# Kernel tuning notes

Hardware: AMD Instinct MI355X
Metric: run time of the kernel (lower is better)

## Reference

```python
import jax, jax.numpy as jnp
import numpy as np

H2 = 1.0  # self.bandwidth = bandwidth**2 with bandwidth=1.0

Q, N, D = 4096, 65536, 32


def setup_inputs() -> dict:
    key = jax.random.key(0)
    k1, k2, k3 = jax.random.split(key, 3)
    X = jax.random.normal(k1, (Q, D), dtype=jnp.float32)
    X_train = jax.random.normal(k2, (N, D), dtype=jnp.float32)
    sample_weight = jax.random.uniform(k3, (N,), dtype=jnp.float32)  # non-negative
    return {"X": X, "X_train": X_train, "sample_weight": sample_weight}


def reference(X, X_train, sample_weight):
    # Brute-force ('standard'/RootTree) KDE: every query sees all train points.
    d = X.shape[-1]
    d2 = (jnp.sum(X * X, axis=-1, keepdims=True)
          + jnp.sum(X_train * X_train, axis=-1)[None, :]
          - 2.0 * (X @ X_train.T))
    # GaussianKernel(diff) = (2*pi)^{-d/2} exp(-||diff||^2 / (2*H2))
    log_k = -0.5 * d2 / H2 - 0.5 * d * jnp.log(jnp.float32(2.0 * np.pi))
    # log( sum_j w_j K_ij / (bw_norm * sum_j w_j) ), bw_norm = H2**(d/2)
    log_num = jax.scipy.special.logsumexp(log_k + jnp.log(sample_weight)[None, :], axis=-1)
    log_norm = 0.5 * d * jnp.log(jnp.float32(H2)) + jnp.log(jnp.sum(sample_weight))
    return log_num - log_norm
```

## Files before the change

kernel.cpp:

```cpp
#include <hip/hip_runtime.h>
#include <math.h>

#define QN 4096
#define NN 65536
#define DD 32

typedef __attribute__((ext_vector_type(8))) _Float16 half8;
typedef __attribute__((ext_vector_type(4))) _Float16 half4v;
typedef __attribute__((ext_vector_type(4))) float floatx4;

#define LOG2E 1.4426950408889634f
#define HALF_D_LOG_2PI 29.40603306254953f

#define ASCALE 2954.6394357789634f
#define BSCALE 4096.0f
#define BIAS_F 1065353216.0f
#define CAPF   1585446912.0f
#define CENTER 0.970656f

__device__ __forceinline__ float fexp_term(float v) {
    v = __builtin_amdgcn_fmed3f(v, 0.0f, CAPF);
    return __int_as_float((int)v);
}


__global__ __launch_bounds__(256) void prep_all(
    const float* __restrict__ X, const float* __restrict__ Xt,
    const float* __restrict__ w, _Float16* __restrict__ Xh,
    float* __restrict__ qn, _Float16* __restrict__ Xth,
    float* __restrict__ c, float* __restrict__ S,
    float* __restrict__ swp) {
    const int b = blockIdx.x;
    if (b < 128) {
        int tid  = b * 256 + threadIdx.x;
        int row  = tid >> 3;
        int part = tid & 7;
        const float4 v = ((const float4*)X)[row * 8 + part];
        float nrm = v.x * v.x + v.y * v.y + v.z * v.z + v.w * v.w;
        nrm += __shfl_xor(nrm, 1);
        nrm += __shfl_xor(nrm, 2);
        nrm += __shfl_xor(nrm, 4);
        half4v h = { (_Float16)(v.x * ASCALE), (_Float16)(v.y * ASCALE),
                     (_Float16)(v.z * ASCALE), (_Float16)(v.w * ASCALE) };
        *(half4v*)(Xh + row * DD + part * 4) = h;
        if (part == 0) qn[row] = 0.5f * nrm;
        if (tid < QN) S[tid] = 0.f;
    } else if (b < 2176) {
        int tid  = (b - 128) * 256 + threadIdx.x;
        int row  = tid >> 3;
        int part = tid & 7;
        const float4 v = ((const float4*)Xt)[row * 8 + part];
        float nrm = v.x * v.x + v.y * v.y + v.z * v.z + v.w * v.w;
        nrm += __shfl_xor(nrm, 1);
        nrm += __shfl_xor(nrm, 2);
        nrm += __shfl_xor(nrm, 4);
        half4v h = { (_Float16)(v.x * BSCALE), (_Float16)(v.y * BSCALE),
                     (_Float16)(v.z * BSCALE), (_Float16)(v.w * BSCALE) };
        *(half4v*)(Xth + row * DD + part * 4) = h;
        if (part == 0)
            c[row] = w[row] * __builtin_amdgcn_exp2f(-0.5f * LOG2E * nrm) * CENTER;
    } else {
        int bid = b - 2176;
        float v = 0.f;
        for (int i = bid * 256 + threadIdx.x; i < NN; i += 64 * 256)
            v += w[i];
        #pragma unroll
        for (int o = 1; o < 64; o <<= 1) v += __shfl_xor(v, o);
        __shared__ float red[4];
        if ((threadIdx.x & 63) == 0) red[threadIdx.x >> 6] = v;
        __syncthreads();
        if (threadIdx.x == 0) swp[bid] = red[0] + red[1] + red[2] + red[3];
    }
}

__global__ __launch_bounds__(256) void kde_main(
    const _Float16* __restrict__ Xh, const _Float16* __restrict__ Xth,
    const float* __restrict__ c, float* __restrict__ S) {
    const int lane   = threadIdx.x & 63;
    const int wave   = threadIdx.x >> 6;
    const int quad   = lane >> 4;
    const int l16    = lane & 15;

    const int b      = blockIdx.x;
    const int xcd    = b & 7;
    const int slot   = b >> 3;
    const int qx     = slot & 15;
    const int strip  = xcd + 8 * (slot >> 4);
    const int m_base = qx * 256 + wave * 64;
    const int n_beg  = strip * 512;

    half8 a0 = *(const half8*)(Xh + (m_base +  0 + l16) * DD + quad * 8);
    half8 a1 = *(const half8*)(Xh + (m_base + 16 + l16) * DD + quad * 8);
    half8 a2 = *(const half8*)(Xh + (m_base + 32 + l16) * DD + quad * 8);
    half8 a3 = *(const half8*)(Xh + (m_base + 48 + l16) * DD + quad * 8);

    float s0[4][4] = {};
    float s1[4][4] = {};
    const floatx4 cbias = {BIAS_F, BIAS_F, BIAS_F, BIAS_F};

    const _Float16* bp = Xth + (size_t)(n_beg + l16) * DD + quad * 8;
    const float*    cp = c + n_beg + l16;

    half8 b0 = *(const half8*)bp;
    half8 b1 = *(const half8*)(bp + 16 * DD);
    float c0 = cp[0];
    float c1 = cp[16];

    for (int it = 0; it < 16; ++it) {
        bp += 32 * DD;
        cp += 32;
        half8 nb0 = *(const half8*)bp;
        half8 nb1 = *(const half8*)(bp + 16 * DD);
        float nc0 = cp[0];
        float nc1 = cp[16];

        floatx4 g00 = __builtin_amdgcn_mfma_f32_16x16x32_f16(a0, b0, cbias, 0, 0, 0);
        floatx4 g10 = __builtin_amdgcn_mfma_f32_16x16x32_f16(a0, b1, cbias, 0, 0, 0);
        floatx4 g01 = __builtin_amdgcn_mfma_f32_16x16x32_f16(a1, b0, cbias, 0, 0, 0);
        floatx4 g11 = __builtin_amdgcn_mfma_f32_16x16x32_f16(a1, b1, cbias, 0, 0, 0);
        floatx4 g02 = __builtin_amdgcn_mfma_f32_16x16x32_f16(a2, b0, cbias, 0, 0, 0);
        floatx4 g12 = __builtin_amdgcn_mfma_f32_16x16x32_f16(a2, b1, cbias, 0, 0, 0);
        floatx4 g03 = __builtin_amdgcn_mfma_f32_16x16x32_f16(a3, b0, cbias, 0, 0, 0);
        floatx4 g13 = __builtin_amdgcn_mfma_f32_16x16x32_f16(a3, b1, cbias, 0, 0, 0);

        #pragma unroll
        for (int r = 0; r < 4; ++r) {
            s0[0][r] += c0 * fexp_term(g00[r]);
            s1[0][r] += c1 * fexp_term(g10[r]);
            s0[1][r] += c0 * fexp_term(g01[r]);
            s1[1][r] += c1 * fexp_term(g11[r]);
            s0[2][r] += c0 * fexp_term(g02[r]);
            s1[2][r] += c1 * fexp_term(g12[r]);
            s0[3][r] += c0 * fexp_term(g03[r]);
            s1[3][r] += c1 * fexp_term(g13[r]);
        }

        b0 = nb0; b1 = nb1; c0 = nc0; c1 = nc1;
    }

    #pragma unroll
    for (int t = 0; t < 4; ++t) {
        #pragma unroll
        for (int r = 0; r < 4; ++r) {
            float v = (t == 0 ? s0[0][r] + s1[0][r] :
                       t == 1 ? s0[1][r] + s1[1][r] :
                       t == 2 ? s0[2][r] + s1[2][r] :
                                s0[3][r] + s1[3][r]);
            v += __shfl_xor(v, 1);
            v += __shfl_xor(v, 2);
            v += __shfl_xor(v, 4);
            v += __shfl_xor(v, 8);
            if (l16 == 0)
                atomicAdd(&S[m_base + t * 16 + quad * 4 + r], v);
        }
    }
}

__global__ void finalize(const float* __restrict__ S, const float* __restrict__ qn,
                         const float* __restrict__ swp, float* __restrict__ out) {
    float pv = swp[threadIdx.x & 63];
    pv += __shfl_xor(pv, 1);
    pv += __shfl_xor(pv, 2);
    pv += __shfl_xor(pv, 4);
    pv += __shfl_xor(pv, 8);
    pv += __shfl_xor(pv, 16);
    pv += __shfl_xor(pv, 32);
    float lsw = logf(pv);
    int i = blockIdx.x * blockDim.x + threadIdx.x;
    out[i] = logf(S[i]) - qn[i] - HALF_D_LOG_2PI - lsw;
}

extern "C" void kernel_launch(void* const* d_in, const int* in_sizes, int n_in,
                              void* d_out, int out_size, void* d_ws, size_t ws_size,
                              hipStream_t stream) {
    const float* X  = (const float*)d_in[0];
    const float* Xt = (const float*)d_in[1];
    const float* w  = (const float*)d_in[2];
    float* out = (float*)d_out;

    char* ws = (char*)d_ws;
    _Float16* Xh   = (_Float16*)(ws);
    _Float16* Xth  = (_Float16*)(ws + 262144);
    float*    c    = (float*)(ws + 4456448);
    float*    qn   = (float*)(ws + 4718592);
    float*    S    = (float*)(ws + 4734976);
    float*    swp  = (float*)(ws + 4751360);

    prep_all<<<2240, 256, 0, stream>>>(X, Xt, w, Xh, qn, Xth, c, S, swp);
    kde_main<<<2048, 256, 0, stream>>>(Xh, Xth, c, S);
    finalize<<<QN / 256, 256, 0, stream>>>(S, qn, swp, out);
}
```

Before: 111.6 us.

## Stage train tiles in double-buffered LDS shared across the block's waves

Each wave used to load its own copy of every train-point tile from global memory. Now the block cooperatively loads 64-row chunks of train points and weights into padded, double-buffered shared memory, and all four waves read their B fragments from there. The aim is to cut redundant global/L2 traffic by a factor of four. In exchange it adds a barrier per chunk and LDS reads, and the padding is there to avoid bank conflicts.

```diff
diff --git a/kernel.cpp b/kernel.cpp
--- a/kernel.cpp
+++ b/kernel.cpp
@@ -22,6 +22,8 @@
     v = __builtin_amdgcn_fmed3f(v, 0.0f, CAPF);
     return __int_as_float((int)v);
 }
+
+#define PS 40
 
 
 __global__ __launch_bounds__(256) void prep_all(
@@ -76,8 +78,9 @@
 __global__ __launch_bounds__(256) void kde_main(
     const _Float16* __restrict__ Xh, const _Float16* __restrict__ Xth,
     const float* __restrict__ c, float* __restrict__ S) {
-    const int lane   = threadIdx.x & 63;
-    const int wave   = threadIdx.x >> 6;
+    const int t      = threadIdx.x;
+    const int lane   = t & 63;
+    const int wave   = t >> 6;
     const int quad   = lane >> 4;
     const int l16    = lane & 15;
 
@@ -89,69 +92,77 @@
     const int m_base = qx * 256 + wave * 64;
     const int n_beg  = strip * 512;
 
+    __shared__ __align__(16) _Float16 bbuf[2][64 * PS];
+    __shared__ float cbuf[2][64];
+
     half8 a0 = *(const half8*)(Xh + (m_base +  0 + l16) * DD + quad * 8);
     half8 a1 = *(const half8*)(Xh + (m_base + 16 + l16) * DD + quad * 8);
     half8 a2 = *(const half8*)(Xh + (m_base + 32 + l16) * DD + quad * 8);
     half8 a3 = *(const half8*)(Xh + (m_base + 48 + l16) * DD + quad * 8);
 
+    const int r   = t >> 2;
+    const int col = (t & 3) * 8;
+    const _Float16* gb = Xth + (size_t)n_beg * DD + t * 8;
+
+    half8 st = *(const half8*)gb;
+    float sc = (t < 64) ? c[n_beg + t] : 0.f;
+    *(half8*)&bbuf[0][r * PS + col] = st;
+    if (t < 64) cbuf[0][t] = sc;
+    __syncthreads();
+
     float s0[4][4] = {};
     float s1[4][4] = {};
     const floatx4 cbias = {BIAS_F, BIAS_F, BIAS_F, BIAS_F};
 
-    const _Float16* bp = Xth + (size_t)(n_beg + l16) * DD + quad * 8;
-    const float*    cp = c + n_beg + l16;
-
-    half8 b0 = *(const half8*)bp;
-    half8 b1 = *(const half8*)(bp + 16 * DD);
-    float c0 = cp[0];
-    float c1 = cp[16];
-
-    for (int it = 0; it < 16; ++it) {
-        bp += 32 * DD;
-        cp += 32;
-        half8 nb0 = *(const half8*)bp;
-        half8 nb1 = *(const half8*)(bp + 16 * DD);
-        float nc0 = cp[0];
-        float nc1 = cp[16];
-
-        floatx4 g00 = __builtin_amdgcn_mfma_f32_16x16x32_f16(a0, b0, cbias, 0, 0, 0);
-        floatx4 g10 = __builtin_amdgcn_mfma_f32_16x16x32_f16(a0, b1, cbias, 0, 0, 0);
-        floatx4 g01 = __builtin_amdgcn_mfma_f32_16x16x32_f16(a1, b0, cbias, 0, 0, 0);
-        floatx4 g11 = __builtin_amdgcn_mfma_f32_16x16x32_f16(a1, b1, cbias, 0, 0, 0);
-        floatx4 g02 = __builtin_amdgcn_mfma_f32_16x16x32_f16(a2, b0, cbias, 0, 0, 0);
-        floatx4 g12 = __builtin_amdgcn_mfma_f32_16x16x32_f16(a2, b1, cbias, 0, 0, 0);
-        floatx4 g03 = __builtin_amdgcn_mfma_f32_16x16x32_f16(a3, b0, cbias, 0, 0, 0);
-        floatx4 g13 = __builtin_amdgcn_mfma_f32_16x16x32_f16(a3, b1, cbias, 0, 0, 0);
+    for (int ch = 0; ch < 8; ++ch) {
+        const int p = ch & 1;
+
+        half8 nst;
+        float nsc = 0.f;
+        if (ch < 7) {
+            gb += 64 * DD;
+            nst = *(const half8*)gb;
+            if (t < 64) nsc = c[n_beg + (ch + 1) * 64 + t];
+        }
 
         #pragma unroll
-        for (int r = 0; r < 4; ++r) {
-            s0[0][r] += c0 * fexp_term(g00[r]);
-            s1[0][r] += c1 * fexp_term(g10[r]);
-            s0[1][r] += c0 * fexp_term(g01[r]);
-            s1[1][r] += c1 * fexp_term(g11[r]);
-            s0[2][r] += c0 * fexp_term(g02[r]);
-            s1[2][r] += c1 * fexp_term(g12[r]);
-            s0[3][r] += c0 * fexp_term(g03[r]);
-            s1[3][r] += c1 * fexp_term(g13[r]);
-        }
-
-        b0 = nb0; b1 = nb1; c0 = nc0; c1 = nc1;
+        for (int j = 0; j < 4; ++j) {
+            half8 bj = *(const half8*)&bbuf[p][(j * 16 + l16) * PS + quad * 8];
+            float cj = cbuf[p][j * 16 + l16];
+
+            floatx4 g0 = __builtin_amdgcn_mfma_f32_16x16x32_f16(a0, bj, cbias, 0, 0, 0);
+            floatx4 g1 = __builtin_amdgcn_mfma_f32_16x16x32_f16(a1, bj, cbias, 0, 0, 0);
+            floatx4 g2 = __builtin_amdgcn_mfma_f32_16x16x32_f16(a2, bj, cbias, 0, 0, 0);
+            floatx4 g3 = __builtin_amdgcn_mfma_f32_16x16x32_f16(a3, bj, cbias, 0, 0, 0);
+
+            float (*s)[4] = (j & 1) ? s1 : s0;
+            #pragma unroll
+            for (int rr = 0; rr < 4; ++rr) {
+                s[0][rr] += cj * fexp_term(g0[rr]);
+                s[1][rr] += cj * fexp_term(g1[rr]);
+                s[2][rr] += cj * fexp_term(g2[rr]);
+                s[3][rr] += cj * fexp_term(g3[rr]);
+            }
+        }
+
+        if (ch < 7) {
+            *(half8*)&bbuf[p ^ 1][r * PS + col] = nst;
+            if (t < 64) cbuf[p ^ 1][t] = nsc;
+        }
+        __syncthreads();
     }
 
     #pragma unroll
-    for (int t = 0; t < 4; ++t) {
+    for (int tt = 0; tt < 4; ++tt) {
         #pragma unroll
-        for (int r = 0; r < 4; ++r) {
-            float v = (t == 0 ? s0[0][r] + s1[0][r] :
-                       t == 1 ? s0[1][r] + s1[1][r] :
-                       t == 2 ? s0[2][r] + s1[2][r] :
-                                s0[3][r] + s1[3][r]);
+        for (int rr = 0; rr < 4; ++rr) {
+            float v = s0[tt][rr] + s1[tt][rr];
             v += __shfl_xor(v, 1);
             v += __shfl_xor(v, 2);
             v += __shfl_xor(v, 4);
             v += __shfl_xor(v, 8);
             if (l16 == 0)
-                atomicAdd(&S[m_base + t * 16 + quad * 4 + r], v);
+                atomicAdd(&S[m_base + tt * 16 + quad * 4 + rr], v);
         }
     }
 }
```

After: 111.6 us. About the same (+0.0%).
